# Performance work log

Measured on AMD Instinct MI355X. Metric: run time of the kernel, lower is better.

Reference implementation:

```python
import jax, jax.numpy as jnp
import numpy as np

B, S, D, H, E, TOPK = 4, 2048, 1024, 1024, 8, 2

def setup_inputs() -> dict:
    key = jax.random.key(0)
    k1, k2, k3 = jax.random.split(key, 3)
    x = jax.random.normal(k1, (B, S, D), dtype=jnp.float32)
    Wg = jax.random.normal(k2, (D, E), dtype=jnp.float32) * (1.0 / np.sqrt(D))
    bg = jnp.zeros((E,), dtype=jnp.float32)
    We = jax.random.normal(k3, (E, D, H), dtype=jnp.float32) * (1.0 / np.sqrt(D))
    be = jnp.zeros((E, H), dtype=jnp.float32)
    return {"x": x, "Wg": Wg, "bg": bg, "We": We, "be": be, "k": TOPK}

def reference(x, Wg, bg, We, be, k):
    # gate logits: [B, S, E]
    logits = jnp.einsum('bsd,de->bse', x, Wg) + bg
    # top-k gating (values, indices along expert axis)
    top_vals, sel = jax.lax.top_k(logits, k)            # [B, S, k]
    weights = jax.nn.softmax(top_vals.astype(jnp.float32), axis=-1).astype(x.dtype)
    # per-token combine weight for each expert: [B, S, E]
    onehot = jax.nn.one_hot(sel, E, dtype=x.dtype)      # [B, S, k, E]
    comb = jnp.einsum('bsk,bske->bse', weights, onehot)
    # all-expert dense outputs (equivalent math to per-expert gather+GEMM+scatter)
    y = jnp.einsum('bsd,edh->besh', x, We) + be[None, :, None, :]  # [B, E, S, H]
    out = jnp.einsum('bse,besh->bsh', comb, y)          # [B, S, H]
    return out
```

## Files before the change

### kernel.cpp

```cpp
#include <hip/hip_runtime.h>
#include <hip/hip_bf16.h>
#include <hip/hip_fp16.h>

#define NTOK 8192
#define DDIM 1024
#define HDIM 1024
#define NEXP 8

typedef __attribute__((ext_vector_type(8))) short short8;
typedef __attribute__((ext_vector_type(4))) float f32x4;
typedef __attribute__((ext_vector_type(4))) unsigned short us4;
typedef __attribute__((ext_vector_type(8))) unsigned short us8;

static __device__ __forceinline__ unsigned short f2bf(float f) {
  union { float f; unsigned u; } v; v.f = f;
  return (unsigned short)((v.u + 0x7fffu + ((v.u >> 16) & 1u)) >> 16);
}

static __device__ __forceinline__ void gload16(const void* g, void* l) {
  __builtin_amdgcn_global_load_lds(
      (const __attribute__((address_space(1))) unsigned int*)g,
      (__attribute__((address_space(3))) unsigned int*)l, 16, 0, 0);
}

__global__ __launch_bounds__(256) void wg_transpose(
    const float* __restrict__ Wg, float* __restrict__ wgT)
{
  const int i = blockIdx.x * 256 + threadIdx.x;
  const int e = i >> 10, d = i & 1023;
  wgT[i] = Wg[d * NEXP + e];
}

__global__ __launch_bounds__(256) void gate_kernel(
    const float* __restrict__ x, const float* __restrict__ wgT,
    const float* __restrict__ bg, unsigned short* __restrict__ xb,
    int* __restrict__ sel, float* __restrict__ wts)
{
  const int token = blockIdx.x * 4 + (threadIdx.x >> 6);
  const int lane = threadIdx.x & 63;
  const float* xr = x + (size_t)token * DDIM;

  float acc[NEXP];
#pragma unroll
  for (int e = 0; e < NEXP; ++e) acc[e] = 0.f;

#pragma unroll
  for (int q = 0; q < 4; ++q) {
    const int d0 = q * 256 + lane * 4;
    const float4 xv = *(const float4*)(xr + d0);
    us4 hb;
    hb.x = f2bf(xv.x); hb.y = f2bf(xv.y); hb.z = f2bf(xv.z); hb.w = f2bf(xv.w);
    *(us4*)(xb + (size_t)token * DDIM + d0) = hb;
#pragma unroll
    for (int e = 0; e < NEXP; ++e) {
      const float4 wv = *(const float4*)(wgT + e * DDIM + d0);
      acc[e] += xv.x * wv.x;
      acc[e] += xv.y * wv.y;
      acc[e] += xv.z * wv.z;
      acc[e] += xv.w * wv.w;
    }
  }

#pragma unroll
  for (int e = 0; e < NEXP; ++e) {
#pragma unroll
    for (int off = 32; off >= 1; off >>= 1)
      acc[e] += __shfl_xor(acc[e], off, 64);
  }

  if (lane == 0) {
    float v[NEXP];
#pragma unroll
    for (int e = 0; e < NEXP; ++e) v[e] = acc[e] + bg[e];
    int i0 = 0; float v0 = v[0];
#pragma unroll
    for (int e = 1; e < NEXP; ++e) if (v[e] > v0) { v0 = v[e]; i0 = e; }
    int i1 = -1; float v1 = -3.4e38f;
#pragma unroll
    for (int e = 0; e < NEXP; ++e) if (e != i0 && v[e] > v1) { v1 = v[e]; i1 = e; }
    const float t = __expf(v1 - v0);
    const float w0 = 1.f / (1.f + t);
    const float w1 = t / (1.f + t);
    sel[token * 2 + 0] = i0;  wts[token * 2 + 0] = w0;
    sel[token * 2 + 1] = i1;  wts[token * 2 + 1] = w1;
  }
}

__global__ __launch_bounds__(256) void route_kernel(
    const int* __restrict__ sel, const float* __restrict__ wts,
    int* __restrict__ counts, int* __restrict__ tlist, float* __restrict__ wlist,
    int* __restrict__ dstrow)
{
  __shared__ int bin[NEXP];
  __shared__ int base[NEXP];
  const int tid = threadIdx.x;
  if (tid < NEXP) bin[tid] = 0;
  __syncthreads();
  const int idx = blockIdx.x * 256 + tid;
  const int e = sel[idx];
  const float w = wts[idx];
  const int rank = atomicAdd(&bin[e], 1);
  __syncthreads();
  if (tid < NEXP) base[tid] = atomicAdd(&counts[tid], bin[tid]);
  __syncthreads();
  const int pos = base[e] + rank;
  tlist[e * NTOK + pos] = idx >> 1;
  wlist[e * NTOK + pos] = w;
  dstrow[e * NTOK + pos] = idx;
}

__global__ __launch_bounds__(256) void transpose_we(
    const float* __restrict__ We, unsigned short* __restrict__ wbt)
{
  const int e = blockIdx.z;
  const int h0 = blockIdx.x * 64;
  const int d0 = blockIdx.y * 128;
  __shared__ float t[128][65];
  const int tx = threadIdx.x;

  {
    const int hc = (tx & 15) * 4;
    const float* src = We + ((size_t)e * DDIM + d0) * HDIM + h0 + hc;
#pragma unroll
    for (int i = 0; i < 8; ++i) {
      const int dr = (tx >> 4) + i * 16;
      const float4 v = *(const float4*)(src + (size_t)dr * HDIM);
      t[dr][hc] = v.x; t[dr][hc + 1] = v.y; t[dr][hc + 2] = v.z; t[dr][hc + 3] = v.w;
    }
  }
  __syncthreads();
  {
    const int dc = (tx & 7) * 16;
#pragma unroll
    for (int i2 = 0; i2 < 2; ++i2) {
      const int hr = (tx >> 3) + i2 * 32;
      us8 o0, o1;
#pragma unroll
      for (int j = 0; j < 8; ++j) ((unsigned short*)&o0)[j] = f2bf(t[dc + j][hr]);
#pragma unroll
      for (int j = 0; j < 8; ++j) ((unsigned short*)&o1)[j] = f2bf(t[dc + 8 + j][hr]);
      unsigned short* dst = wbt + ((size_t)e * HDIM + h0 + hr) * DDIM + d0 + dc;
      *(us8*)dst = o0;
      *(us8*)(dst + 8) = o1;
    }
  }
}

__global__ __launch_bounds__(512, 2) void moe_gemm(
    const unsigned short* __restrict__ xb,
    const unsigned short* __restrict__ wbt,
    const float* __restrict__ be,
    const int* __restrict__ counts,
    const int* __restrict__ tlist,
    const float* __restrict__ wlist,
    const int* __restrict__ dstrow,
    __half* __restrict__ yb)
{
  const int e = blockIdx.z;
  const int cnt = counts[e];
  const int tile = blockIdx.y;
  if (tile * 256 >= cnt) return;
  const int n0 = blockIdx.x * 256;

  __shared__ unsigned short As[256 * 64];
  __shared__ unsigned short Bs[256 * 64];

  const int tid = threadIdx.x;
  const int lane = tid & 63;
  const int wv = tid >> 6;
  const int wm = wv >> 2;
  const int wn = wv & 3;

  const int rA = tid >> 3;
  const int kbA = (tid & 7) << 4;
  int aOff[4]; int bOff[4]; int ldsO[4];
#pragma unroll
  for (int q = 0; q < 4; ++q) {
    const int r = q * 64 + rA;
    int trow = tile * 256 + r;
    trow = trow < cnt ? trow : cnt - 1;
    const int tok = tlist[e * NTOK + trow];
    const int kbs = kbA ^ ((r & 7) << 4);
    aOff[q] = tok * DDIM + (kbs >> 1);
    bOff[q] = (e * HDIM + n0 + r) * DDIM + (kbs >> 1);
    ldsO[q] = r * 64 + (kbA >> 1);
  }

  f32x4 acc[8][4];
#pragma unroll
  for (int m = 0; m < 8; ++m)
#pragma unroll
    for (int n = 0; n < 4; ++n)
      acc[m][n] = (f32x4){0.f, 0.f, 0.f, 0.f};

  for (int kt = 0; kt < DDIM / 64; ++kt) {
    __syncthreads();
#pragma unroll
    for (int q = 0; q < 4; ++q) gload16(xb + aOff[q] + kt * 64, &As[ldsO[q]]);
#pragma unroll
    for (int q = 0; q < 4; ++q) gload16(wbt + bOff[q] + kt * 64, &Bs[ldsO[q]]);
    __syncthreads();

#pragma unroll
    for (int kk = 0; kk < 2; ++kk) {
      const int kb = kk * 64 + ((lane >> 4) << 4);
      short8 af[8], bfr[4];
#pragma unroll
      for (int m = 0; m < 8; ++m) {
        const int r = wm * 128 + m * 16 + (lane & 15);
        af[m] = *(const short8*)((const char*)As + r * 128 + (kb ^ ((r & 7) << 4)));
      }
#pragma unroll
      for (int n = 0; n < 4; ++n) {
        const int r = wn * 64 + n * 16 + (lane & 15);
        bfr[n] = *(const short8*)((const char*)Bs + r * 128 + (kb ^ ((r & 7) << 4)));
      }
#pragma unroll
      for (int m = 0; m < 8; ++m)
#pragma unroll
        for (int n = 0; n < 4; ++n)
          acc[m][n] = __builtin_amdgcn_mfma_f32_16x16x32_bf16(af[m], bfr[n], acc[m][n], 0, 0, 0);
    }
  }

  const int rbase = wm * 128 + ((lane >> 4) << 2);
  const int cb = lane & 15;
  float bev[4];
#pragma unroll
  for (int n = 0; n < 4; ++n) bev[n] = be[e * HDIM + n0 + wn * 64 + n * 16 + cb];
#pragma unroll
  for (int m = 0; m < 8; ++m) {
#pragma unroll
    for (int r4 = 0; r4 < 4; ++r4) {
      const int trow = tile * 256 + rbase + m * 16 + r4;
      if (trow < cnt) {
        const int drow = dstrow[e * NTOK + trow];
        const float w = wlist[e * NTOK + trow];
        __half* yrow = yb + (size_t)drow * HDIM + n0 + wn * 64 + cb;
#pragma unroll
        for (int n = 0; n < 4; ++n)
          yrow[n * 16] = __float2half(w * (acc[m][n][r4] + bev[n]));
      }
    }
  }
}

__global__ __launch_bounds__(256) void combine_kernel(
    const __half* __restrict__ yb, float* __restrict__ out)
{
  const int g = blockIdx.x * 256 + threadIdx.x;
  const int tok = g >> 7;
  const int h0 = (g & 127) * 8;
  const short8 p0 = *(const short8*)(yb + ((size_t)tok * 2) * HDIM + h0);
  const short8 p1 = *(const short8*)(yb + ((size_t)tok * 2 + 1) * HDIM + h0);
  float r[8];
#pragma unroll
  for (int j = 0; j < 8; ++j) {
    __half a = *(const __half*)&((const short*)&p0)[j];
    __half b = *(const __half*)&((const short*)&p1)[j];
    r[j] = __half2float(a) + __half2float(b);
  }
  float* o = out + (size_t)tok * HDIM + h0;
  *(float4*)o = (float4){r[0], r[1], r[2], r[3]};
  *(float4*)(o + 4) = (float4){r[4], r[5], r[6], r[7]};
}

extern "C" void kernel_launch(void* const* d_in, const int* in_sizes, int n_in,
                              void* d_out, int out_size, void* d_ws, size_t ws_size,
                              hipStream_t stream)
{
  const float* x  = (const float*)d_in[0];
  const float* Wg = (const float*)d_in[1];
  const float* bg = (const float*)d_in[2];
  const float* We = (const float*)d_in[3];
  const float* be = (const float*)d_in[4];

  char* ws = (char*)d_ws;
  int*   counts = (int*)ws;
  int*   tlist  = (int*)(ws + 256);
  float* wlist  = (float*)(ws + 256 + NEXP * NTOK * 4);
  int*   dstrow = (int*)(ws + 256 + 2 * NEXP * NTOK * 4);
  int*   sel    = (int*)(ws + 256 + 3 * NEXP * NTOK * 4);
  float* wts    = (float*)(ws + 256 + 3 * NEXP * NTOK * 4 + 2 * NTOK * 4);
  float* wgT    = (float*)(ws + 0x180000);
  unsigned short* xb  = (unsigned short*)(ws + (1 << 21));
  unsigned short* wbt = (unsigned short*)(ws + (1 << 21) + (size_t)NTOK * DDIM * 2);
  __half* yb = (__half*)(ws + (1 << 21) + 2 * (size_t)NTOK * DDIM * 2);
  float* out = (float*)d_out;

  hipMemsetAsync(counts, 0, 256, stream);

  wg_transpose<<<32, 256, 0, stream>>>(Wg, wgT);
  gate_kernel<<<NTOK / 4, 256, 0, stream>>>(x, wgT, bg, xb, sel, wts);
  route_kernel<<<2 * NTOK / 256, 256, 0, stream>>>(sel, wts, counts, tlist, wlist, dstrow);
  transpose_we<<<dim3(HDIM / 64, DDIM / 128, NEXP), 256, 0, stream>>>(We, wbt);
  moe_gemm<<<dim3(HDIM / 256, NTOK / 256, NEXP), 512, 0, stream>>>(
      xb, wbt, be, counts, tlist, wlist, dstrow, yb);
  combine_kernel<<<NTOK * HDIM / 8 / 256, 256, 0, stream>>>(yb, out);
}
```

Before: 222.5 us.

## Shrink MoE GEMM N-tile to 128, raise occupancy, stage gate weights in LDS

```diff
diff --git a/kernel.cpp b/kernel.cpp
--- a/kernel.cpp
+++ b/kernel.cpp
@@ -36,53 +36,66 @@
     const float* __restrict__ bg, unsigned short* __restrict__ xb,
     int* __restrict__ sel, float* __restrict__ wts)
 {
-  const int token = blockIdx.x * 4 + (threadIdx.x >> 6);
-  const int lane = threadIdx.x & 63;
-  const float* xr = x + (size_t)token * DDIM;
-
-  float acc[NEXP];
-#pragma unroll
-  for (int e = 0; e < NEXP; ++e) acc[e] = 0.f;
-
-#pragma unroll
-  for (int q = 0; q < 4; ++q) {
-    const int d0 = q * 256 + lane * 4;
-    const float4 xv = *(const float4*)(xr + d0);
-    us4 hb;
-    hb.x = f2bf(xv.x); hb.y = f2bf(xv.y); hb.z = f2bf(xv.z); hb.w = f2bf(xv.w);
-    *(us4*)(xb + (size_t)token * DDIM + d0) = hb;
+  __shared__ float wg[NEXP * DDIM];
+  const int tid = threadIdx.x;
+#pragma unroll
+  for (int i = 0; i < 8; ++i) {
+    const int o = (i * 256 + tid) * 4;
+    *(float4*)&wg[o] = *(const float4*)&wgT[o];
+  }
+  __syncthreads();
+
+  const int wave = tid >> 6;
+  const int lane = tid & 63;
+
+  for (int t = 0; t < 4; ++t) {
+    const int token = blockIdx.x * 16 + wave * 4 + t;
+    const float* xr = x + (size_t)token * DDIM;
+
+    float acc[NEXP];
+#pragma unroll
+    for (int e = 0; e < NEXP; ++e) acc[e] = 0.f;
+
+#pragma unroll
+    for (int q = 0; q < 4; ++q) {
+      const int d0 = q * 256 + lane * 4;
+      const float4 xv = *(const float4*)(xr + d0);
+      us4 hb;
+      hb.x = f2bf(xv.x); hb.y = f2bf(xv.y); hb.z = f2bf(xv.z); hb.w = f2bf(xv.w);
+      *(us4*)(xb + (size_t)token * DDIM + d0) = hb;
+#pragma unroll
+      for (int e = 0; e < NEXP; ++e) {
+        const float4 wv = *(const float4*)&wg[e * DDIM + d0];
+        acc[e] += xv.x * wv.x;
+        acc[e] += xv.y * wv.y;
+        acc[e] += xv.z * wv.z;
+        acc[e] += xv.w * wv.w;
+      }
+    }
+
 #pragma unroll
     for (int e = 0; e < NEXP; ++e) {
-      const float4 wv = *(const float4*)(wgT + e * DDIM + d0);
-      acc[e] += xv.x * wv.x;
-      acc[e] += xv.y * wv.y;
-      acc[e] += xv.z * wv.z;
-      acc[e] += xv.w * wv.w;
-    }
-  }
-
-#pragma unroll
-  for (int e = 0; e < NEXP; ++e) {
-#pragma unroll
-    for (int off = 32; off >= 1; off >>= 1)
-      acc[e] += __shfl_xor(acc[e], off, 64);
-  }
-
-  if (lane == 0) {
-    float v[NEXP];
-#pragma unroll
-    for (int e = 0; e < NEXP; ++e) v[e] = acc[e] + bg[e];
-    int i0 = 0; float v0 = v[0];
-#pragma unroll
-    for (int e = 1; e < NEXP; ++e) if (v[e] > v0) { v0 = v[e]; i0 = e; }
-    int i1 = -1; float v1 = -3.4e38f;
-#pragma unroll
-    for (int e = 0; e < NEXP; ++e) if (e != i0 && v[e] > v1) { v1 = v[e]; i1 = e; }
-    const float t = __expf(v1 - v0);
-    const float w0 = 1.f / (1.f + t);
-    const float w1 = t / (1.f + t);
-    sel[token * 2 + 0] = i0;  wts[token * 2 + 0] = w0;
-    sel[token * 2 + 1] = i1;  wts[token * 2 + 1] = w1;
+#pragma unroll
+      for (int off = 32; off >= 1; off >>= 1)
+        acc[e] += __shfl_xor(acc[e], off, 64);
+    }
+
+    if (lane == 0) {
+      float v[NEXP];
+#pragma unroll
+      for (int e = 0; e < NEXP; ++e) v[e] = acc[e] + bg[e];
+      int i0 = 0; float v0 = v[0];
+#pragma unroll
+      for (int e = 1; e < NEXP; ++e) if (v[e] > v0) { v0 = v[e]; i0 = e; }
+      int i1 = -1; float v1 = -3.4e38f;
+#pragma unroll
+      for (int e = 0; e < NEXP; ++e) if (e != i0 && v[e] > v1) { v1 = v[e]; i1 = e; }
+      const float tt = __expf(v1 - v0);
+      const float w0 = 1.f / (1.f + tt);
+      const float w1 = tt / (1.f + tt);
+      sel[token * 2 + 0] = i0;  wts[token * 2 + 0] = w0;
+      sel[token * 2 + 1] = i1;  wts[token * 2 + 1] = w1;
+    }
   }
 }
 
@@ -146,7 +159,7 @@
   }
 }
 
-__global__ __launch_bounds__(512, 2) void moe_gemm(
+__global__ __launch_bounds__(512, 4) void moe_gemm(
     const unsigned short* __restrict__ xb,
     const unsigned short* __restrict__ wbt,
     const float* __restrict__ be,
@@ -160,20 +173,22 @@
   const int cnt = counts[e];
   const int tile = blockIdx.y;
   if (tile * 256 >= cnt) return;
-  const int n0 = blockIdx.x * 256;
+  const int n0 = blockIdx.x * 128;
 
   __shared__ unsigned short As[256 * 64];
-  __shared__ unsigned short Bs[256 * 64];
+  __shared__ unsigned short Bs[128 * 64];
 
   const int tid = threadIdx.x;
   const int lane = tid & 63;
   const int wv = tid >> 6;
-  const int wm = wv >> 2;
-  const int wn = wv & 3;
+  const int wm = wv >> 1;
+  const int wn = wv & 1;
 
   const int rA = tid >> 3;
   const int kbA = (tid & 7) << 4;
-  int aOff[4]; int bOff[4]; int ldsO[4];
+  const unsigned short* aSrc[4];
+  const unsigned short* bSrc[2];
+  int ldsA[4]; int ldsB[2];
 #pragma unroll
   for (int q = 0; q < 4; ++q) {
     const int r = q * 64 + rA;
@@ -181,14 +196,20 @@
     trow = trow < cnt ? trow : cnt - 1;
     const int tok = tlist[e * NTOK + trow];
     const int kbs = kbA ^ ((r & 7) << 4);
-    aOff[q] = tok * DDIM + (kbs >> 1);
-    bOff[q] = (e * HDIM + n0 + r) * DDIM + (kbs >> 1);
-    ldsO[q] = r * 64 + (kbA >> 1);
-  }
-
-  f32x4 acc[8][4];
-#pragma unroll
-  for (int m = 0; m < 8; ++m)
+    aSrc[q] = xb + (size_t)tok * DDIM + (kbs >> 1);
+    ldsA[q] = r * 64 + (kbA >> 1);
+  }
+#pragma unroll
+  for (int q = 0; q < 2; ++q) {
+    const int r = q * 64 + rA;
+    const int kbs = kbA ^ ((r & 7) << 4);
+    bSrc[q] = wbt + ((size_t)e * HDIM + n0 + r) * DDIM + (kbs >> 1);
+    ldsB[q] = r * 64 + (kbA >> 1);
+  }
+
+  f32x4 acc[4][4];
+#pragma unroll
+  for (int m = 0; m < 4; ++m)
 #pragma unroll
     for (int n = 0; n < 4; ++n)
       acc[m][n] = (f32x4){0.f, 0.f, 0.f, 0.f};
@@ -196,18 +217,18 @@
   for (int kt = 0; kt < DDIM / 64; ++kt) {
     __syncthreads();
 #pragma unroll
-    for (int q = 0; q < 4; ++q) gload16(xb + aOff[q] + kt * 64, &As[ldsO[q]]);
-#pragma unroll
-    for (int q = 0; q < 4; ++q) gload16(wbt + bOff[q] + kt * 64, &Bs[ldsO[q]]);
+    for (int q = 0; q < 4; ++q) gload16(aSrc[q] + kt * 64, &As[ldsA[q]]);
+#pragma unroll
+    for (int q = 0; q < 2; ++q) gload16(bSrc[q] + kt * 64, &Bs[ldsB[q]]);
     __syncthreads();
 
 #pragma unroll
     for (int kk = 0; kk < 2; ++kk) {
       const int kb = kk * 64 + ((lane >> 4) << 4);
-      short8 af[8], bfr[4];
-#pragma unroll
-      for (int m = 0; m < 8; ++m) {
-        const int r = wm * 128 + m * 16 + (lane & 15);
+      short8 af[4], bfr[4];
+#pragma unroll
+      for (int m = 0; m < 4; ++m) {
+        const int r = wm * 64 + m * 16 + (lane & 15);
         af[m] = *(const short8*)((const char*)As + r * 128 + (kb ^ ((r & 7) << 4)));
       }
 #pragma unroll
@@ -216,20 +237,20 @@
         bfr[n] = *(const short8*)((const char*)Bs + r * 128 + (kb ^ ((r & 7) << 4)));
       }
 #pragma unroll
-      for (int m = 0; m < 8; ++m)
+      for (int m = 0; m < 4; ++m)
 #pragma unroll
         for (int n = 0; n < 4; ++n)
           acc[m][n] = __builtin_amdgcn_mfma_f32_16x16x32_bf16(af[m], bfr[n], acc[m][n], 0, 0, 0);
     }
   }
 
-  const int rbase = wm * 128 + ((lane >> 4) << 2);
+  const int rbase = wm * 64 + ((lane >> 4) << 2);
   const int cb = lane & 15;
   float bev[4];
 #pragma unroll
   for (int n = 0; n < 4; ++n) bev[n] = be[e * HDIM + n0 + wn * 64 + n * 16 + cb];
 #pragma unroll
-  for (int m = 0; m < 8; ++m) {
+  for (int m = 0; m < 4; ++m) {
 #pragma unroll
     for (int r4 = 0; r4 < 4; ++r4) {
       const int trow = tile * 256 + rbase + m * 16 + r4;
@@ -291,10 +312,10 @@
   hipMemsetAsync(counts, 0, 256, stream);
 
   wg_transpose<<<32, 256, 0, stream>>>(Wg, wgT);
-  gate_kernel<<<NTOK / 4, 256, 0, stream>>>(x, wgT, bg, xb, sel, wts);
+  gate_kernel<<<NTOK / 16, 256, 0, stream>>>(x, wgT, bg, xb, sel, wts);
   route_kernel<<<2 * NTOK / 256, 256, 0, stream>>>(sel, wts, counts, tlist, wlist, dstrow);
   transpose_we<<<dim3(HDIM / 64, DDIM / 128, NEXP), 256, 0, stream>>>(We, wbt);
-  moe_gemm<<<dim3(HDIM / 256, NTOK / 256, NEXP), 512, 0, stream>>>(
+  moe_gemm<<<dim3(HDIM / 128, NTOK / 256, NEXP), 512, 0, stream>>>(
       xb, wbt, be, counts, tlist, wlist, dstrow, yb);
   combine_kernel<<<NTOK * HDIM / 8 / 256, 256, 0, stream>>>(yb, out);
 }
```

Result: faster. 201.5 us (-9.5%).
